# Kernel tuning notes

Hardware: AMD Instinct MI355X
Metric: run time of the kernel (lower is better)

## Reference

```python
import jax, jax.numpy as jnp
import numpy as np

MARGIN = 1.0
REL_W = 0.3


def setup_inputs() -> dict:
    key = jax.random.key(0)
    ks = jax.random.split(key, 12)
    D = 256
    inp = {
        'support': jax.random.normal(ks[0], (16, 5, 1, 2, D), jnp.float32),
        'support_negative': jax.random.normal(ks[1], (16, 5, 1, 2, D), jnp.float32),
        'query': jax.random.normal(ks[2], (16, 128, 1, 2, D), jnp.float32),
        'negative': jax.random.normal(ks[3], (16, 128, 1, 2, D), jnp.float32),
        # PatternLearner conv weights (kaiming-ish scale), squeezed to 2-D since all convs are (1,3)/(1,1)
        'w1': jax.random.normal(ks[4], (128, 3), jnp.float32) * np.float32(np.sqrt(2.0 / 3.0)),
        'b1': jnp.zeros((128,), jnp.float32),
        'w2': jax.random.normal(ks[5], (64, 128), jnp.float32) * np.float32(np.sqrt(2.0 / 128.0)),
        'b2': jnp.zeros((64,), jnp.float32),
        'w3': jax.random.normal(ks[6], (32, 64), jnp.float32) * np.float32(np.sqrt(2.0 / 64.0)),
        'b3': jnp.zeros((32,), jnp.float32),
        'w4': jax.random.normal(ks[7], (1, 32), jnp.float32) * np.float32(np.sqrt(2.0 / 32.0)),
        'b4': jnp.zeros((1,), jnp.float32),
    }
    return inp


def _pattern_learner(x, w1, b1, w2, b2, w3, b3, w4, b4):
    # x: [B, N, 1, 3, D] -> torch does view+transpose -> conv2d(1,3) over the length-3 axis,
    # then 1x1 channel convs; equivalent to per-(n,d) contractions.
    h = x[:, :, 0]                                   # [B, N, 3, D]
    h = jnp.einsum('bnld,ol->bndo', h, w1) + b1      # [B, N, D, 128]
    h = jax.nn.relu(h)
    h = jax.nn.relu(jnp.einsum('bndi,oi->bndo', h, w2) + b2)
    h = jax.nn.relu(jnp.einsum('bndi,oi->bndo', h, w3) + b3)
    h = jnp.einsum('bndi,oi->bndo', h, w4) + b4      # [B, N, D, 1]
    return h[..., 0]                                 # [B, N, D]


def _concat_relation(pairs, rel):
    # pairs: [B, N, 1, 2, D]; rel: [B, 1, 1, 1, D]
    B, N, C, _, D = pairs.shape
    head = pairs[:, :, :, 0, :]
    tail = pairs[:, :, :, 1, :]
    relb = jnp.broadcast_to(rel[:, :, :, 0, :], (B, N, C, D))
    # torch cat order (relation, head, tail) then reindex [1,0,2] -> (head, relation, tail)
    return jnp.stack([head, relb, tail], axis=3)     # [B, N, 1, 3, D]


def _pattern_match(q, s):
    # q: [B, Nq, D], s: [B, 1, D] -> -L2 norm
    return -jnp.linalg.norm(q - s, axis=-1)


def reference(support, support_negative, query, negative, w1, b1, w2, b2, w3, b3, w4, b4):
    B, num_q = query.shape[0], query.shape[1]
    num_n = negative.shape[1]
    # get_relation(mean=True): tail - head averaged over the few support pairs
    rel = jnp.mean(support[:, :, :, 1, :] - support[:, :, :, 0, :], axis=1, keepdims=True)
    rel = rel[:, :, :, None, :]                      # [B, 1, 1, 1, D]

    sup_t = _concat_relation(support, rel)
    supn_t = _concat_relation(support_negative, rel)
    qry_t = _concat_relation(query, rel)
    neg_t = _concat_relation(negative, rel)

    pl = lambda x: _pattern_learner(x, w1, b1, w2, b2, w3, b3, w4, b4)
    spt_pos = pl(sup_t)                              # [B, few, D]
    spt_neg = pl(supn_t)                             # [B, num_sn, D]
    qry = pl(jnp.concatenate([qry_t, neg_t], axis=1))  # [B, num_q+num_n, D]

    # aggregator == 'relation': prototypes are per-task means of positive support patterns
    proto = jnp.mean(spt_pos, axis=1)                # [B, D]
    spt_pos_m = proto[:, None, :]                    # [B, 1, D]
    spt_neg_m = jnp.mean(spt_neg, axis=1, keepdims=True)

    qry_pos = _pattern_match(qry, spt_pos_m)         # [B, Nq]
    qry_neg = _pattern_match(qry, spt_neg_m)

    # relation_score (vectorized): mean L2 distance to all OTHER tasks' prototypes, negated
    dists = jnp.linalg.norm(qry[:, :, None, :] - proto[None, None, :, :], axis=-1)  # [B, Nq, B]
    idx = jnp.arange(B)
    self_d = dists[idx, :, idx]                      # [B, Nq]
    relation_score = -(dists.sum(-1) - self_d) / (B - 1)

    # margin loss on the true-query slice
    pos_score = _pattern_match(qry[:, :num_q], spt_pos_m)
    neg_score = _pattern_match(qry[:, :num_q], spt_neg_m)
    pos_ = jnp.mean(pos_score)
    neg_ = jnp.mean(neg_score)
    delta_loss = jnp.maximum(0.0, pos_ - neg_ + MARGIN)

    score = jnp.stack([qry_pos, qry_neg], axis=-1).reshape(-1, 2)
    row = jnp.concatenate([jnp.zeros((num_q,), jnp.int32), jnp.ones((num_n,), jnp.int32)])
    y_query = jnp.broadcast_to(row, (B, num_q + num_n)).reshape(-1)

    delta = qry_pos - qry_neg - REL_W * relation_score  # vbm + relation branch
    p_score = delta[:, :num_q]
    n_score = delta[:, num_q:]
    return (score, y_query, p_score, n_score, delta_loss)
```

## Files before the change

kernel.cpp:

```cpp
#include <hip/hip_runtime.h>
#include <hip/hip_bf16.h>

typedef _Float16 f16;
typedef f16 f16x8 __attribute__((ext_vector_type(8)));
typedef f16 f16x2 __attribute__((ext_vector_type(2)));
typedef float f32x4 __attribute__((ext_vector_type(4)));
typedef unsigned int u32;

#define MFMA16(a, b, c) __builtin_amdgcn_mfma_f32_16x16x32_f16((a), (b), (c), 0, 0, 0)

__device__ __forceinline__ u32 pkrz(float a, float b) {
    auto r = __builtin_amdgcn_cvt_pkrtz(a, b);
    return __builtin_bit_cast(u32, r);
}
__device__ __forceinline__ u32 pkmax0(u32 x) {
    f16x2 h = __builtin_bit_cast(f16x2, x);
    f16x2 z = {(f16)0.f, (f16)0.f};
    f16x2 m = __builtin_elementwise_max(h, z);
    return __builtin_bit_cast(u32, m);
}
__device__ __forceinline__ u32 pkrelu(float a, float b) {
    return pkmax0(pkrz(a, b));
}

union U8 { f16x8 h; u32 w[4]; };

#define OFF_Y      4096

__device__ __forceinline__ int b_of(int e) {
    if (e < 20480) return e / 1280;
    if (e < 40960) return (e - 20480) / 1280;
    return (e - 40960) >> 16;
}

__global__ __launch_bounds__(256, 2) void k_main(
    const float* __restrict__ sup, const float* __restrict__ supn,
    const float* __restrict__ qry, const float* __restrict__ neg,
    const float* __restrict__ w1, const float* __restrict__ b1p,
    const float* __restrict__ w2, const float* __restrict__ w3,
    const float* __restrict__ w4, const float* __restrict__ b2p,
    const float* __restrict__ b3p, const float* __restrict__ b4p,
    float* __restrict__ ws)
{
    __shared__ __align__(16) f16x8 w2lds[16 * 64];
    __shared__ __align__(16) f16x8 wpk[13 * 64];
    __shared__ uint2 stage[4][64];
    __shared__ float relb[2][256];
    float* wsY = ws + OFF_Y;

    int tid = threadIdx.x, wv = tid >> 6, lane = tid & 63;
    int g = lane >> 4, col = lane & 15;
    const f32x4 zero4 = {0.f, 0.f, 0.f, 0.f};

    int blkbase = blockIdx.x * 1024;
    int rb0 = b_of(blkbase), rb1 = b_of(blkbase + 1023);

    #pragma unroll
    for (int k = 0; k < 2; k++) {
        int bb = k ? rb1 : rb0;
        float acc = 0.f;
        #pragma unroll
        for (int n = 0; n < 5; n++) {
            const float* base = sup + ((bb * 5 + n) * 2) * 256 + tid;
            acc += base[256] - base[0];
        }
        relb[k][tid] = acc * 0.2f;
    }

    #pragma unroll
    for (int i = 0; i < 4; i++) {
        int id = tid + 256 * i;
        int f = id >> 6, ln = id & 63;
        int gg = ln >> 4, cr = ln & 15;
        int t = f >> 2, kk = f & 3, out = t * 16 + cr;
        U8 v;
        #pragma unroll
        for (int i2 = 0; i2 < 8; i2++) {
            int u = (2 * kk + (i2 >> 2)) * 16 + gg * 4 + (i2 & 3);
            v.h[i2] = (f16)w2[out * 128 + u];
        }
        w2lds[id] = v.h;
    }
    for (int id = tid; id < 13 * 64; id += 256) {
        int fi = id >> 6, ln = id & 63;
        int gg = ln >> 4, cr = ln & 15, kb = gg * 8;
        U8 v;
        if (fi < 8) {
            int out = fi * 16 + cr;
            #pragma unroll
            for (int i2 = 0; i2 < 8; i2++) {
                int k = kb + i2;
                v.h[i2] = (f16)((k < 3) ? w1[out * 3 + k] : (k == 3 ? b1p[out] : 0.f));
            }
        } else if (fi < 12) {
            int f = fi - 8; int t = f >> 1, kk = f & 1; int out = t * 16 + cr;
            #pragma unroll
            for (int i2 = 0; i2 < 8; i2++) {
                int u = (2 * kk + (i2 >> 2)) * 16 + gg * 4 + (i2 & 3);
                v.h[i2] = (f16)w3[out * 64 + u];
            }
        } else {
            #pragma unroll
            for (int i2 = 0; i2 < 8; i2++) {
                int u = (i2 >> 2) * 16 + gg * 4 + (i2 & 3);
                v.h[i2] = (f16)((cr == 0) ? w4[u] : 0.f);
            }
        }
        wpk[id] = v.h;
    }
    __syncthreads();

    f16x8 w1f[8], w3f[4], w4f;
    #pragma unroll
    for (int f = 0; f < 8; f++) w1f[f] = wpk[f * 64 + lane];
    #pragma unroll
    for (int f = 0; f < 4; f++) w3f[f] = wpk[(8 + f) * 64 + lane];
    w4f = wpk[12 * 64 + lane];

    f32x4 bias2[4], bias3[2];
    #pragma unroll
    for (int t = 0; t < 4; t++) {
        int o = t * 16 + g * 4;
        bias2[t] = (f32x4){b2p[o], b2p[o + 1], b2p[o + 2], b2p[o + 3]};
    }
    #pragma unroll
    for (int t = 0; t < 2; t++) {
        int o = t * 16 + g * 4;
        bias3[t] = (f32x4){b3p[o], b3p[o + 1], b3p[o + 2], b3p[o + 3]};
    }
    float b4v = b4p[0];

    int base = blkbase + wv * 256;

    for (int it = 0; it < 4; ++it) {
        int e = base + it * 64 + lane;
        const float* hp; int bb, dd;
        if (e < 40960) {
            int e2 = (e < 20480) ? e : e - 20480;
            bb = e2 / 1280; int r = e2 - bb * 1280;
            int n = r >> 8; dd = r & 255;
            const float* srcp = (e < 20480) ? sup : supn;
            hp = srcp + ((bb * 5 + n) * 2) * 256 + dd;
        } else {
            int e2 = e - 40960;
            bb = e2 >> 16; int r = e2 & 65535, m = r >> 8; dd = r & 255;
            hp = (m < 128) ? (qry + ((bb * 128 + m) * 2) * 256 + dd)
                           : (neg + ((bb * 128 + (m - 128)) * 2) * 256 + dd);
        }
        float x0 = hp[0], x2 = hp[256];
        float x1 = relb[(bb == rb0) ? 0 : 1][dd];
        stage[wv][lane] = make_uint2(pkrz(x0, x1), pkrz(x2, 1.0f));

        #pragma unroll
        for (int jp = 0; jp < 2; ++jp) {
            U8 b1a, b1b;
            #pragma unroll
            for (int q = 0; q < 4; q++) { b1a.w[q] = 0u; b1b.w[q] = 0u; }
            if (g == 0) {
                uint2 sa = stage[wv][(2 * jp) * 16 + col];
                uint2 sb = stage[wv][(2 * jp + 1) * 16 + col];
                b1a.w[0] = sa.x; b1a.w[1] = sa.y;
                b1b.w[0] = sb.x; b1b.w[1] = sb.y;
            }

            f32x4 c1a[8], c1b[8];
            #pragma unroll
            for (int t = 0; t < 8; t++) {
                c1a[t] = MFMA16(w1f[t], b1a.h, zero4);
                c1b[t] = MFMA16(w1f[t], b1b.h, zero4);
            }

            U8 b2fa[4], b2fb[4];
            #pragma unroll
            for (int kk = 0; kk < 4; kk++) {
                b2fa[kk].w[0] = pkrelu(c1a[2 * kk][0],     c1a[2 * kk][1]);
                b2fa[kk].w[1] = pkrelu(c1a[2 * kk][2],     c1a[2 * kk][3]);
                b2fa[kk].w[2] = pkrelu(c1a[2 * kk + 1][0], c1a[2 * kk + 1][1]);
                b2fa[kk].w[3] = pkrelu(c1a[2 * kk + 1][2], c1a[2 * kk + 1][3]);
                b2fb[kk].w[0] = pkrelu(c1b[2 * kk][0],     c1b[2 * kk][1]);
                b2fb[kk].w[1] = pkrelu(c1b[2 * kk][2],     c1b[2 * kk][3]);
                b2fb[kk].w[2] = pkrelu(c1b[2 * kk + 1][0], c1b[2 * kk + 1][1]);
                b2fb[kk].w[3] = pkrelu(c1b[2 * kk + 1][2], c1b[2 * kk + 1][3]);
            }

            f32x4 c2a[4], c2b[4];
            #pragma unroll
            for (int t = 0; t < 4; t++) {
                f32x4 ca = bias2[t], cb = bias2[t];
                #pragma unroll
                for (int kk = 0; kk < 4; kk++) {
                    f16x8 wfr = w2lds[(t * 4 + kk) * 64 + lane];
                    ca = MFMA16(wfr, b2fa[kk].h, ca);
                    cb = MFMA16(wfr, b2fb[kk].h, cb);
                }
                c2a[t] = ca; c2b[t] = cb;
            }

            U8 b3fa[2], b3fb[2];
            #pragma unroll
            for (int kk = 0; kk < 2; kk++) {
                b3fa[kk].w[0] = pkrelu(c2a[2 * kk][0],     c2a[2 * kk][1]);
                b3fa[kk].w[1] = pkrelu(c2a[2 * kk][2],     c2a[2 * kk][3]);
                b3fa[kk].w[2] = pkrelu(c2a[2 * kk + 1][0], c2a[2 * kk + 1][1]);
                b3fa[kk].w[3] = pkrelu(c2a[2 * kk + 1][2], c2a[2 * kk + 1][3]);
                b3fb[kk].w[0] = pkrelu(c2b[2 * kk][0],     c2b[2 * kk][1]);
                b3fb[kk].w[1] = pkrelu(c2b[2 * kk][2],     c2b[2 * kk][3]);
                b3fb[kk].w[2] = pkrelu(c2b[2 * kk + 1][0], c2b[2 * kk + 1][1]);
                b3fb[kk].w[3] = pkrelu(c2b[2 * kk + 1][2], c2b[2 * kk + 1][3]);
            }

            f32x4 c3a[2], c3b[2];
            #pragma unroll
            for (int t = 0; t < 2; t++) {
                f32x4 ca = bias3[t], cb = bias3[t];
                #pragma unroll
                for (int kk = 0; kk < 2; kk++) {
                    ca = MFMA16(w3f[t * 2 + kk], b3fa[kk].h, ca);
                    cb = MFMA16(w3f[t * 2 + kk], b3fb[kk].h, cb);
                }
                c3a[t] = ca; c3b[t] = cb;
            }

            U8 b4fa, b4fb;
            b4fa.w[0] = pkrelu(c3a[0][0], c3a[0][1]);
            b4fa.w[1] = pkrelu(c3a[0][2], c3a[0][3]);
            b4fa.w[2] = pkrelu(c3a[1][0], c3a[1][1]);
            b4fa.w[3] = pkrelu(c3a[1][2], c3a[1][3]);
            b4fb.w[0] = pkrelu(c3b[0][0], c3b[0][1]);
            b4fb.w[1] = pkrelu(c3b[0][2], c3b[0][3]);
            b4fb.w[2] = pkrelu(c3b[1][0], c3b[1][1]);
            b4fb.w[3] = pkrelu(c3b[1][2], c3b[1][3]);

            f32x4 c4a = MFMA16(w4f, b4fa.h, zero4);
            f32x4 c4b = MFMA16(w4f, b4fb.h, zero4);
            if (lane < 16) {
                wsY[base + it * 64 + (2 * jp) * 16 + lane]     = c4a[0] + b4v;
                wsY[base + it * 64 + (2 * jp + 1) * 16 + lane] = c4b[0] + b4v;
            }
        }
    }
}

__global__ __launch_bounds__(256) void k_scores(float* __restrict__ ws, float* __restrict__ out)
{
    __shared__ float proto[16][256];
    __shared__ float snegs[256];
    const float* y = ws + OFF_Y;
    int tid = threadIdx.x;
    int row0 = blockIdx.x * 4;
    int b = row0 >> 8;

    #pragma unroll
    for (int i = 0; i < 16; i++) {
        int idx = tid + 256 * i;
        int c = idx >> 8, d = idx & 255;
        float s = 0.f;
        #pragma unroll
        for (int n = 0; n < 5; n++) s += y[c * 1280 + n * 256 + d];
        proto[c][d] = s * 0.2f;
    }
    {
        float s = 0.f;
        #pragma unroll
        for (int n = 0; n < 5; n++) s += y[20480 + b * 1280 + n * 256 + tid];
        snegs[tid] = s * 0.2f;
    }
    __syncthreads();

    int row = row0 + (tid >> 6);
    int lane = tid & 63;
    int m = row & 255;
    const float* q = y + 40960 + row * 256;
    float q0 = q[lane], q1 = q[lane + 64], q2 = q[lane + 128], q3 = q[lane + 192];

    float s[17];
    #pragma unroll
    for (int c = 0; c < 16; c++) {
        float d0 = q0 - proto[c][lane],       d1 = q1 - proto[c][lane + 64];
        float d2 = q2 - proto[c][lane + 128], d3 = q3 - proto[c][lane + 192];
        s[c] = d0 * d0 + d1 * d1 + d2 * d2 + d3 * d3;
    }
    {
        float d0 = q0 - snegs[lane],       d1 = q1 - snegs[lane + 64];
        float d2 = q2 - snegs[lane + 128], d3 = q3 - snegs[lane + 192];
        s[16] = d0 * d0 + d1 * d1 + d2 * d2 + d3 * d3;
    }
    #pragma unroll
    for (int off = 32; off > 0; off >>= 1) {
        #pragma unroll
        for (int c = 0; c < 17; c++) s[c] += __shfl_xor(s[c], off, 64);
    }
    float sumd = 0.f, selfd = 0.f;
    #pragma unroll
    for (int c = 0; c < 16; c++) {
        float dc = sqrtf(s[c]);
        sumd += dc;
        if (c == b) selfd = dc;
    }
    float qpos = -selfd;
    float qneg = -sqrtf(s[16]);
    float relation = -(sumd - selfd) * (1.f / 15.f);
    float delta = qpos - qneg - 0.3f * relation;

    if (lane == 0) {
        out[2 * row] = qpos;
        out[2 * row + 1] = qneg;
        out[8192 + row] = (m < 128) ? 0.f : 1.f;
        if (m < 128) out[12288 + b * 128 + m] = delta;
        else         out[14336 + b * 128 + (m - 128)] = delta;
    }
}

__global__ __launch_bounds__(256) void k_final(float* __restrict__ out)
{
    __shared__ float red[2][256];
    int t = threadIdx.x;
    float sp = 0.f, sn = 0.f;
    #pragma unroll
    for (int i = 0; i < 8; i++) {
        int idx = t + 256 * i;
        int b = idx >> 7, m = idx & 127;
        int row = b * 256 + m;
        sp += out[2 * row];
        sn += out[2 * row + 1];
    }
    red[0][t] = sp; red[1][t] = sn;
    __syncthreads();
    #pragma unroll
    for (int off = 128; off > 0; off >>= 1) {
        if (t < off) { red[0][t] += red[0][t + off]; red[1][t] += red[1][t + off]; }
        __syncthreads();
    }
    if (t == 0) {
        float v = (red[0][0] - red[1][0]) * (1.f / 2048.f) + 1.f;
        out[16384] = fmaxf(v, 0.f);
    }
}

extern "C" void kernel_launch(void* const* d_in, const int* in_sizes, int n_in,
                              void* d_out, int out_size, void* d_ws, size_t ws_size,
                              hipStream_t stream)
{
    const float* sup  = (const float*)d_in[0];
    const float* supn = (const float*)d_in[1];
    const float* qry  = (const float*)d_in[2];
    const float* neg  = (const float*)d_in[3];
    const float* w1   = (const float*)d_in[4];
    const float* b1   = (const float*)d_in[5];
    const float* w2   = (const float*)d_in[6];
    const float* b2   = (const float*)d_in[7];
    const float* w3   = (const float*)d_in[8];
    const float* b3   = (const float*)d_in[9];
    const float* w4   = (const float*)d_in[10];
    const float* b4   = (const float*)d_in[11];
    float* ws  = (float*)d_ws;
    float* out = (float*)d_out;

    k_main  <<<1064, 256, 0, stream>>>(sup, supn, qry, neg, w1, b1, w2, w3, w4, b2, b3, b4, ws);
    k_scores<<<1024, 256, 0, stream>>>(ws, out);
    k_final <<<1,    256, 0, stream>>>(out);
}
```

Baseline: 130.8 us.

## Precompute prototype means in a separate kernel and process more rows per block

Adds a small kernel that computes the per-task support and negative-support means once into the workspace. The scoring kernel no longer recomputes all 16 prototypes per block: it loads them directly and handles 16 query rows per block instead of 4, cutting the block count fourfold. This removes large redundant global/L2 reads, at the cost of one extra kernel launch and less parallelism in the scoring kernel.

```diff
diff --git a/kernel.cpp b/kernel.cpp
--- a/kernel.cpp
+++ b/kernel.cpp
@@ -26,6 +26,8 @@
 union U8 { f16x8 h; u32 w[4]; };
 
 #define OFF_Y      4096
+#define OFF_PROTO  1093632
+#define OFF_SNEG   1097728
 
 __device__ __forceinline__ int b_of(int e) {
     if (e < 20480) return e / 1280;
@@ -241,73 +243,80 @@
     }
 }
 
+__global__ void k_means(float* __restrict__ ws)
+{
+    int idx = blockIdx.x * 256 + threadIdx.x;
+    int b = idx >> 8, d = idx & 255;
+    const float* y = ws + OFF_Y;
+    float sp = 0.f, sn = 0.f;
+    #pragma unroll
+    for (int n = 0; n < 5; n++) {
+        sp += y[b * 1280 + n * 256 + d];
+        sn += y[20480 + b * 1280 + n * 256 + d];
+    }
+    ws[OFF_PROTO + idx] = sp * 0.2f;
+    ws[OFF_SNEG + idx] = sn * 0.2f;
+}
+
 __global__ __launch_bounds__(256) void k_scores(float* __restrict__ ws, float* __restrict__ out)
 {
     __shared__ float proto[16][256];
     __shared__ float snegs[256];
     const float* y = ws + OFF_Y;
     int tid = threadIdx.x;
-    int row0 = blockIdx.x * 4;
+    int row0 = blockIdx.x * 16;
     int b = row0 >> 8;
 
     #pragma unroll
-    for (int i = 0; i < 16; i++) {
-        int idx = tid + 256 * i;
-        int c = idx >> 8, d = idx & 255;
-        float s = 0.f;
-        #pragma unroll
-        for (int n = 0; n < 5; n++) s += y[c * 1280 + n * 256 + d];
-        proto[c][d] = s * 0.2f;
-    }
-    {
-        float s = 0.f;
-        #pragma unroll
-        for (int n = 0; n < 5; n++) s += y[20480 + b * 1280 + n * 256 + tid];
-        snegs[tid] = s * 0.2f;
-    }
+    for (int i = 0; i < 16; i++)
+        proto[i][tid] = ws[OFF_PROTO + i * 256 + tid];
+    snegs[tid] = ws[OFF_SNEG + b * 256 + tid];
     __syncthreads();
 
-    int row = row0 + (tid >> 6);
-    int lane = tid & 63;
-    int m = row & 255;
-    const float* q = y + 40960 + row * 256;
-    float q0 = q[lane], q1 = q[lane + 64], q2 = q[lane + 128], q3 = q[lane + 192];
-
-    float s[17];
-    #pragma unroll
-    for (int c = 0; c < 16; c++) {
-        float d0 = q0 - proto[c][lane],       d1 = q1 - proto[c][lane + 64];
-        float d2 = q2 - proto[c][lane + 128], d3 = q3 - proto[c][lane + 192];
-        s[c] = d0 * d0 + d1 * d1 + d2 * d2 + d3 * d3;
-    }
-    {
-        float d0 = q0 - snegs[lane],       d1 = q1 - snegs[lane + 64];
-        float d2 = q2 - snegs[lane + 128], d3 = q3 - snegs[lane + 192];
-        s[16] = d0 * d0 + d1 * d1 + d2 * d2 + d3 * d3;
-    }
-    #pragma unroll
-    for (int off = 32; off > 0; off >>= 1) {
-        #pragma unroll
-        for (int c = 0; c < 17; c++) s[c] += __shfl_xor(s[c], off, 64);
-    }
-    float sumd = 0.f, selfd = 0.f;
-    #pragma unroll
-    for (int c = 0; c < 16; c++) {
-        float dc = sqrtf(s[c]);
-        sumd += dc;
-        if (c == b) selfd = dc;
-    }
-    float qpos = -selfd;
-    float qneg = -sqrtf(s[16]);
-    float relation = -(sumd - selfd) * (1.f / 15.f);
-    float delta = qpos - qneg - 0.3f * relation;
-
-    if (lane == 0) {
-        out[2 * row] = qpos;
-        out[2 * row + 1] = qneg;
-        out[8192 + row] = (m < 128) ? 0.f : 1.f;
-        if (m < 128) out[12288 + b * 128 + m] = delta;
-        else         out[14336 + b * 128 + (m - 128)] = delta;
+    int wv = tid >> 6, lane = tid & 63;
+
+    for (int r = 0; r < 4; r++) {
+        int row = row0 + wv * 4 + r;
+        int m = row & 255;
+        const float* q = y + 40960 + row * 256;
+        float q0 = q[lane], q1 = q[lane + 64], q2 = q[lane + 128], q3 = q[lane + 192];
+
+        float s[17];
+        #pragma unroll
+        for (int c = 0; c < 16; c++) {
+            float d0 = q0 - proto[c][lane],       d1 = q1 - proto[c][lane + 64];
+            float d2 = q2 - proto[c][lane + 128], d3 = q3 - proto[c][lane + 192];
+            s[c] = d0 * d0 + d1 * d1 + d2 * d2 + d3 * d3;
+        }
+        {
+            float d0 = q0 - snegs[lane],       d1 = q1 - snegs[lane + 64];
+            float d2 = q2 - snegs[lane + 128], d3 = q3 - snegs[lane + 192];
+            s[16] = d0 * d0 + d1 * d1 + d2 * d2 + d3 * d3;
+        }
+        #pragma unroll
+        for (int off = 32; off > 0; off >>= 1) {
+            #pragma unroll
+            for (int c = 0; c < 17; c++) s[c] += __shfl_xor(s[c], off, 64);
+        }
+        float sumd = 0.f, selfd = 0.f;
+        #pragma unroll
+        for (int c = 0; c < 16; c++) {
+            float dc = sqrtf(s[c]);
+            sumd += dc;
+            if (c == b) selfd = dc;
+        }
+        float qpos = -selfd;
+        float qneg = -sqrtf(s[16]);
+        float relation = -(sumd - selfd) * (1.f / 15.f);
+        float delta = qpos - qneg - 0.3f * relation;
+
+        if (lane == 0) {
+            out[2 * row] = qpos;
+            out[2 * row + 1] = qneg;
+            out[8192 + row] = (m < 128) ? 0.f : 1.f;
+            if (m < 128) out[12288 + b * 128 + m] = delta;
+            else         out[14336 + b * 128 + (m - 128)] = delta;
+        }
     }
 }
 
@@ -357,6 +366,7 @@
     float* out = (float*)d_out;
 
     k_main  <<<1064, 256, 0, stream>>>(sup, supn, qry, neg, w1, b1, w2, w3, w4, b2, b3, b4, ws);
-    k_scores<<<1024, 256, 0, stream>>>(ws, out);
+    k_means <<<16,   256, 0, stream>>>(ws);
+    k_scores<<<256,  256, 0, stream>>>(ws, out);
     k_final <<<1,    256, 0, stream>>>(out);
 }
```

Result: slower. 133.4 us (+2.0%).
